# Kernel tuning notes

Hardware: AMD Instinct MI355X
Metric: run time of the kernel (lower is better)

## Reference

```python
import jax, jax.numpy as jnp
import numpy as np

N_NODES = 10000
N_EDGES = 160000
MUL = 128            # channel multiplicity
N_SPECIES = 4        # node_attrs scalars
N_RADIAL = 8         # edge_feats scalars
AVG_NEIGH = 16.0
SQRT3 = 1.7320508075688772


def setup_inputs() -> dict:
    key = jax.random.key(0)
    ks = jax.random.split(key, 16)
    inp = {}
    inp['node_attrs'] = jax.random.uniform(ks[0], (N_NODES, N_SPECIES), dtype=jnp.float32)
    inp['node_feats'] = jax.random.normal(ks[1], (N_NODES, MUL * 4), dtype=jnp.float32)  # 128x0e + 128x1o
    inp['edge_attrs'] = jax.random.normal(ks[2], (N_EDGES, 4), dtype=jnp.float32)        # 1x0e + 1x1o (SH lmax=1)
    inp['edge_feats'] = jax.random.normal(ks[3], (N_EDGES, N_RADIAL), dtype=jnp.float32)
    inp['edge_index'] = jax.random.randint(ks[4], (2, N_EDGES), 0, N_NODES, dtype=jnp.int32)
    # linear_up: per-l mixing (o3.Linear on 128x0e+128x1o)
    inp['W_up0'] = jax.random.normal(ks[5], (MUL, MUL), dtype=jnp.float32)
    inp['W_up1'] = jax.random.normal(ks[6], (MUL, MUL), dtype=jnp.float32)
    # radial MLP [8, 64, 64, 512] (conv_tp.weight_numel = 4 instructions * 128)
    inp['W_mlp1'] = jax.random.normal(ks[7], (N_RADIAL, 64), dtype=jnp.float32)
    inp['W_mlp2'] = jax.random.normal(ks[8], (64, 64), dtype=jnp.float32)
    inp['W_mlp3'] = jax.random.normal(ks[9], (64, 4 * MUL), dtype=jnp.float32)
    # linear: irreps_mid.simplify() = 256x0e + 256x1o -> 128x0e + 128x1o
    inp['W_lin0'] = jax.random.normal(ks[10], (2 * MUL, MUL), dtype=jnp.float32)
    inp['W_lin1'] = jax.random.normal(ks[11], (2 * MUL, MUL), dtype=jnp.float32)
    # skip_tp: FullyConnectedTensorProduct(target, 4x0e -> target), uvw weights per l
    inp['W_skip0'] = jax.random.normal(ks[12], (MUL, N_SPECIES, MUL), dtype=jnp.float32)
    inp['W_skip1'] = jax.random.normal(ks[13], (MUL, N_SPECIES, MUL), dtype=jnp.float32)
    inp['update_coeff_param'] = jnp.zeros((1,), dtype=jnp.float32)
    return inp


def reference(node_attrs, node_feats, edge_attrs, edge_feats, edge_index,
              W_up0, W_up1, W_mlp1, W_mlp2, W_mlp3, W_lin0, W_lin1,
              W_skip0, W_skip1, update_coeff_param):
    N = node_feats.shape[0]
    # split node feats into irrep blocks: scalars [N,128], vectors [N,128,3]
    s = node_feats[:, :MUL]
    v = node_feats[:, MUL:].reshape(N, MUL, 3)
    # linear_up (o3.Linear, fan-in normalized)
    inv_up = 1.0 / jnp.sqrt(jnp.float32(MUL))
    s = (s @ W_up0) * inv_up
    v = jnp.einsum('nui,uw->nwi', v, W_up1) * inv_up
    # radial MLP -> per-edge TP weights (e3nn FullyConnectedNet style, fan-in normalized, silu)
    h = jax.nn.silu((edge_feats @ W_mlp1) / jnp.sqrt(jnp.float32(N_RADIAL)))
    h = jax.nn.silu((h @ W_mlp2) / jnp.sqrt(jnp.float32(64)))
    tpw = (h @ W_mlp3) / jnp.sqrt(jnp.float32(64))  # [E, 512]
    # instruction order (sorted by output irrep): 0e*0e->0e, 1o*1o->0e, 0e*1o->1o, 1o*0e->1o
    w_a, w_b, w_c, w_d = tpw[:, :MUL], tpw[:, MUL:2*MUL], tpw[:, 2*MUL:3*MUL], tpw[:, 3*MUL:]
    sender, receiver = edge_index[0], edge_index[1]
    xs = s[sender]          # [E,128] gather
    xv = v[sender]          # [E,128,3]
    ea_s = edge_attrs[:, :1]    # [E,1]
    ea_v = edge_attrs[:, 1:4]   # [E,3]
    # CG tensor-product messages ('uvu', component norm)
    m0 = w_a * xs * ea_s                                        # 0e x 0e -> 0e
    m1 = w_b * (jnp.einsum('eui,ei->eu', xv, ea_v) / SQRT3)      # 1o x 1o -> 0e
    m2 = (w_c * xs)[:, :, None] * ea_v[:, None, :]               # 0e x 1o -> 1o
    m3 = w_d[:, :, None] * xv * ea_s[:, :, None]                 # 1o x 0e -> 1o
    ms = jnp.concatenate([m0, m1], axis=1)                       # [E,256]
    mv = jnp.concatenate([m2, m3], axis=1)                       # [E,256,3]
    # scatter-sum to receiver nodes
    Ms = jax.ops.segment_sum(ms, receiver, num_segments=N)       # [N,256]
    Mv = jax.ops.segment_sum(mv, receiver, num_segments=N)       # [N,256,3]
    # linear (256x0e+256x1o -> 128x0e+128x1o), divided by avg_num_neighbors
    inv_lin = 1.0 / (jnp.sqrt(jnp.float32(2 * MUL)) * AVG_NEIGH)
    S = (Ms @ W_lin0) * inv_lin                                  # [N,128]
    V = jnp.einsum('nui,uw->nwi', Mv, W_lin1) * inv_lin          # [N,128,3]
    # skip_tp: FullyConnectedTensorProduct(message, node_attrs) with uvw weights
    inv_sk = 1.0 / jnp.sqrt(jnp.float32(MUL * N_SPECIES))
    sc_s = jnp.einsum('nu,nv,uvw->nw', S, node_attrs, W_skip0) * inv_sk
    sc_v = jnp.einsum('nui,nv,uvw->nwi', V, node_attrs, W_skip1) * inv_sk
    # residual stream mixing (sc=False branch)
    c = jax.nn.sigmoid(update_coeff_param)                       # [1]
    c_old = jax.lax.rsqrt(c * c + 1.0)
    c_new = c * c_old
    S = c_old * S + c_new * sc_s
    V = c_old * V + c_new * sc_v
    # reshape_irreps: [N, mul, 1 + 3]
    out = jnp.concatenate([S[:, :, None], V], axis=-1)           # [N,128,4]
    return out
```

## Files before the change

### kernel.cpp

```cpp
#include <hip/hip_runtime.h>

#define MUL 128

typedef __attribute__((ext_vector_type(8))) short bf16x8;
typedef __attribute__((ext_vector_type(4))) short bf16x4;
typedef __attribute__((ext_vector_type(4))) float f32x4;

__device__ __constant__ float kINV_UP   = 0.08838834764831845f;
__device__ __constant__ float kINV_L1   = 0.35355339059327373f;
__device__ __constant__ float kINV_L2   = 0.125f;
__device__ __constant__ float kINV_L3   = 0.125f;
__device__ __constant__ float kINV_LIN  = 0.00390625f;
__device__ __constant__ float kINV_SK   = 0.044194173824159216f;
__device__ __constant__ float kINV_SQ3  = 0.5773502691896258f;

static __device__ __forceinline__ short f2bf(float f) {
  unsigned u = __float_as_uint(f);
  unsigned r = (u + 0x7FFFu + ((u >> 16) & 1u)) >> 16;
  return (short)r;
}

__global__ __launch_bounds__(256) void k_cvt(
    const float* __restrict__ W_up0, const float* __restrict__ W_up1,
    const float* __restrict__ W_lin0, const float* __restrict__ W_lin1,
    const float* __restrict__ W_sk0, const float* __restrict__ W_sk1,
    const float* __restrict__ W_mlp2, const float* __restrict__ W_mlp3,
    short* __restrict__ W0T, short* __restrict__ W1T,
    short* __restrict__ Wl0T, short* __restrict__ Wl1T,
    short* __restrict__ Wsk0T, short* __restrict__ Wsk1T,
    short* __restrict__ W2T, short* __restrict__ W3T) {
  int id = blockIdx.x * 256 + threadIdx.x;
  if (id < 16384) {
    int w = id >> 7, u = id & 127;
    W0T[id] = f2bf(W_up0[u * 128 + w]);
    return;
  }
  id -= 16384;
  if (id < 16384) {
    int w = id >> 7, u = id & 127;
    W1T[id] = f2bf(W_up1[u * 128 + w]);
    return;
  }
  id -= 16384;
  if (id < 32768) {
    int w = id >> 8, u = id & 255;
    Wl0T[id] = f2bf(W_lin0[u * 128 + w]);
    return;
  }
  id -= 32768;
  if (id < 32768) {
    int w = id >> 8, u = id & 255;
    Wl1T[id] = f2bf(W_lin1[u * 128 + w]);
    return;
  }
  id -= 32768;
  if (id < 65536) {
    int w = id >> 9, k = id & 511;
    int v = k >> 7, u = k & 127;
    Wsk0T[id] = f2bf(W_sk0[(u * 4 + v) * 128 + w]);
    return;
  }
  id -= 65536;
  if (id < 65536) {
    int w = id >> 9, k = id & 511;
    int v = k >> 7, u = k & 127;
    Wsk1T[id] = f2bf(W_sk1[(u * 4 + v) * 128 + w]);
    return;
  }
  id -= 65536;
  if (id < 4096) {
    int c = id >> 6, k = id & 63;
    W2T[id] = f2bf(W_mlp2[k * 64 + c]);
    return;
  }
  id -= 4096;
  if (id < 32768) {
    int c = id >> 6, k = id & 63;
    W3T[id] = f2bf(W_mlp3[k * 512 + c]);
  }
}

__global__ __launch_bounds__(256) void k_up_mfma(const float* __restrict__ nf,
                                                 const short* __restrict__ W0T,
                                                 const short* __restrict__ W1T,
                                                 float* __restrict__ s_up,
                                                 float* __restrict__ v_up,
                                                 int N) {
  __shared__ __align__(16) short lsA[4][16][136];
  const int nb = blockIdx.x * 16;
  const int t = threadIdx.x;

  for (int base = t * 8; base < 16 * 512; base += 256 * 8) {
    int n = base >> 9, j0 = base & 511;
    float vals[8];
    if (nb + n < N) {
      float4 q0 = *reinterpret_cast<const float4*>(nf + (size_t)(nb + n) * 512 + j0);
      float4 q1 = *reinterpret_cast<const float4*>(nf + (size_t)(nb + n) * 512 + j0 + 4);
      vals[0] = q0.x; vals[1] = q0.y; vals[2] = q0.z; vals[3] = q0.w;
      vals[4] = q1.x; vals[5] = q1.y; vals[6] = q1.z; vals[7] = q1.w;
    } else {
#pragma unroll
      for (int e = 0; e < 8; ++e) vals[e] = 0.f;
    }
#pragma unroll
    for (int e = 0; e < 8; ++e) {
      int idx = j0 + e;
      if (idx < 128) {
        lsA[0][n][idx] = f2bf(vals[e]);
      } else {
        unsigned q = idx - 128;
        unsigned u = q / 3u;
        unsigned i = q - u * 3u;
        lsA[1 + i][n][u] = f2bf(vals[e]);
      }
    }
  }
  __syncthreads();

  const int c = t >> 6;
  const int lane = t & 63;
  const int col = lane & 15;
  const int g = lane >> 4;

  const short* WT = c ? W1T : W0T;

  bf16x8 af[4];
#pragma unroll
  for (int kk = 0; kk < 4; ++kk)
    af[kk] = *reinterpret_cast<const bf16x8*>(&lsA[c][col][kk * 32 + g * 8]);

#pragma unroll
  for (int nt = 0; nt < 8; ++nt) {
    f32x4 acc = {0.f, 0.f, 0.f, 0.f};
#pragma unroll
    for (int kk = 0; kk < 4; ++kk) {
      bf16x8 bf = *reinterpret_cast<const bf16x8*>(&WT[(size_t)(nt * 16 + col) * 128 + kk * 32 + g * 8]);
      acc = __builtin_amdgcn_mfma_f32_16x16x32_bf16(af[kk], bf, acc, 0, 0, 0);
    }
#pragma unroll
    for (int r = 0; r < 4; ++r) {
      int nd = nb + g * 4 + r;
      if (nd < N) {
        float val = acc[r] * kINV_UP;
        if (c == 0) s_up[(size_t)nd * 128 + nt * 16 + col] = val;
        else        v_up[(size_t)nd * 384 + (c - 1) * 128 + nt * 16 + col] = val;
      }
    }
  }
}

__global__ void k_count(const int* __restrict__ eidx, int* __restrict__ cnt, int E) {
  int e = blockIdx.x * 256 + threadIdx.x;
  if (e < E) atomicAdd(&cnt[eidx[E + e]], 1);
}

__global__ __launch_bounds__(1024) void k_scan(const int* __restrict__ cnt,
                                               int* __restrict__ offs,
                                               int* __restrict__ cursor, int N) {
  __shared__ int part[1024];
  const int t = threadIdx.x;
  int CH = (N + 1023) >> 10;
  if (CH > 16) CH = 16;
  const int base = t * CH;
  int loc[16];
  int s = 0;
  for (int i = 0; i < CH; ++i) {
    int idx = base + i;
    loc[i] = (idx < N) ? cnt[idx] : 0;
    s += loc[i];
  }
  part[t] = s;
  __syncthreads();
  for (int off = 1; off < 1024; off <<= 1) {
    int v = part[t];
    int add = (t >= off) ? part[t - off] : 0;
    __syncthreads();
    part[t] = v + add;
    __syncthreads();
  }
  int excl = part[t] - s;
  for (int i = 0; i < CH; ++i) {
    int idx = base + i;
    if (idx < N) { offs[idx] = excl; cursor[idx] = excl; }
    excl += loc[i];
  }
  if (t == 1023) offs[N] = part[1023];
}

__global__ void k_scatter(const int* __restrict__ eidx, int* __restrict__ cursor,
                          int* __restrict__ sorted, int E) {
  int e = blockIdx.x * 256 + threadIdx.x;
  if (e < E) {
    int r = eidx[E + e];
    int p = atomicAdd(&cursor[r], 1);
    sorted[p] = e;
  }
}

__global__ __launch_bounds__(256) void k_mlp(
    const int* __restrict__ sorted, const float* __restrict__ ef,
    const float* __restrict__ W1, const short* __restrict__ W2T,
    const short* __restrict__ W3T, unsigned* __restrict__ tpw2, int E) {
  __shared__ float sef[64][12];
  __shared__ float sW1[8 * 64];
  __shared__ __align__(16) short sW2T[64][72];
  __shared__ __align__(16) short sh1[64][72];
  __shared__ __align__(16) short sh2[64][72];

  const int pb = blockIdx.x * 64;
  const int t = threadIdx.x;

  for (int i = t * 4; i < 512; i += 1024)
    *reinterpret_cast<float4*>(&sW1[i]) = *reinterpret_cast<const float4*>(W1 + i);
  for (int i = t * 8; i < 4096; i += 2048) {
    int r = i >> 6, c = i & 63;
    *reinterpret_cast<bf16x8*>(&sW2T[r][c]) = *reinterpret_cast<const bf16x8*>(&W2T[r * 64 + c]);
  }
  if (t < 128) {
    int le = t >> 1, half = t & 1;
    int p = pb + le;
    float4 q = {0.f, 0.f, 0.f, 0.f};
    if (p < E) {
      int eid = sorted[p];
      q = *reinterpret_cast<const float4*>(ef + (size_t)eid * 8 + half * 4);
    }
    *reinterpret_cast<float4*>(&sef[le][half * 4]) = q;
  }
  __syncthreads();

  {
    const int e = t & 63, cg = t >> 6;
    float acc[16] = {};
#pragma unroll
    for (int k = 0; k < 8; ++k) {
      float x = sef[e][k];
#pragma unroll
      for (int j = 0; j < 16; ++j) acc[j] += x * sW1[k * 64 + cg * 16 + j];
    }
#pragma unroll
    for (int j = 0; j < 16; ++j) {
      float a = acc[j] * kINV_L1;
      sh1[e][cg * 16 + j] = f2bf(a / (1.f + __expf(-a)));
    }
  }
  __syncthreads();

  const int lane = t & 63, w = t >> 6;
  const int li = lane & 15, g = lane >> 4;
  const int e = w * 16 + li;

  {
    bf16x8 b0 = *reinterpret_cast<const bf16x8*>(&sh1[e][g * 8]);
    bf16x8 b1 = *reinterpret_cast<const bf16x8*>(&sh1[e][32 + g * 8]);
#pragma unroll
    for (int ct = 0; ct < 4; ++ct) {
      bf16x8 a0 = *reinterpret_cast<const bf16x8*>(&sW2T[ct * 16 + li][g * 8]);
      bf16x8 a1 = *reinterpret_cast<const bf16x8*>(&sW2T[ct * 16 + li][32 + g * 8]);
      f32x4 acc = {0.f, 0.f, 0.f, 0.f};
      acc = __builtin_amdgcn_mfma_f32_16x16x32_bf16(a0, b0, acc, 0, 0, 0);
      acc = __builtin_amdgcn_mfma_f32_16x16x32_bf16(a1, b1, acc, 0, 0, 0);
      bf16x4 h;
#pragma unroll
      for (int r = 0; r < 4; ++r) {
        float a = acc[r] * kINV_L2;
        h[r] = f2bf(a / (1.f + __expf(-a)));
      }
      *reinterpret_cast<bf16x4*>(&sh2[e][ct * 16 + g * 4]) = h;
    }
  }
  __syncthreads();

  {
    const int p = pb + e;
    bf16x8 b0 = *reinterpret_cast<const bf16x8*>(&sh2[e][g * 8]);
    bf16x8 b1 = *reinterpret_cast<const bf16x8*>(&sh2[e][32 + g * 8]);
#pragma unroll 4
    for (int rt = 0; rt < 16; ++rt) {
      const int rowA = rt * 16 + li;
      bf16x8 a0 = *reinterpret_cast<const bf16x8*>(&W3T[(size_t)rowA * 64 + g * 8]);
      bf16x8 a1 = *reinterpret_cast<const bf16x8*>(&W3T[(size_t)rowA * 64 + 32 + g * 8]);
      bf16x8 a2 = *reinterpret_cast<const bf16x8*>(&W3T[(size_t)(rowA + 256) * 64 + g * 8]);
      bf16x8 a3 = *reinterpret_cast<const bf16x8*>(&W3T[(size_t)(rowA + 256) * 64 + 32 + g * 8]);
      f32x4 accA = {0.f, 0.f, 0.f, 0.f};
      f32x4 accB = {0.f, 0.f, 0.f, 0.f};
      accA = __builtin_amdgcn_mfma_f32_16x16x32_bf16(a0, b0, accA, 0, 0, 0);
      accA = __builtin_amdgcn_mfma_f32_16x16x32_bf16(a1, b1, accA, 0, 0, 0);
      accB = __builtin_amdgcn_mfma_f32_16x16x32_bf16(a2, b0, accB, 0, 0, 0);
      accB = __builtin_amdgcn_mfma_f32_16x16x32_bf16(a3, b1, accB, 0, 0, 0);
      if (p < E) {
        uint4 d;
        unsigned* dp = &d.x;
#pragma unroll
        for (int r = 0; r < 4; ++r) {
          unsigned lo = (unsigned)(unsigned short)f2bf(accA[r] * kINV_L3);
          unsigned hi = (unsigned)(unsigned short)f2bf(accB[r] * kINV_L3);
          dp[r] = lo | (hi << 16);
        }
        *reinterpret_cast<uint4*>(&tpw2[(size_t)p * 256 + rt * 16 + g * 4]) = d;
      }
    }
  }
}

__global__ __launch_bounds__(256) void k_gather(
    const int* __restrict__ sorted, const int* __restrict__ offs,
    const unsigned* __restrict__ tpw2, const float* __restrict__ eattr,
    const int* __restrict__ eidx,
    const float* __restrict__ s_up, const float* __restrict__ v_up,
    float* __restrict__ Ms, float* __restrict__ Mv, int N, int SB) {
  const int t = threadIdx.x;
  const int vside = blockIdx.x >= SB;
  const int nb = (vside ? blockIdx.x - SB : blockIdx.x) * 4;
  const int n = nb + (t >> 6);
  if (n >= N) return;
  const int l = t & 63;
  const int u0 = l * 2;

  float aMs0 = 0.f, aMs1 = 0.f;
  float aV[3][2] = {};

  const int e0 = offs[n], e1 = offs[n + 1];

  if (!vside) {
    for (int p = e0; p < e1; ++p) {
      int eid = sorted[p];
      int snd = eidx[eid];
      float4 ea = *reinterpret_cast<const float4*>(eattr + (size_t)eid * 4);
      uint2 q = *reinterpret_cast<const uint2*>(tpw2 + (size_t)p * 256 + u0);
      float2 xs = *reinterpret_cast<const float2*>(s_up + (size_t)snd * 128 + u0);
      float tA0 = __uint_as_float(q.x << 16);
      float tB0 = __uint_as_float(q.x & 0xFFFF0000u);
      float tA1 = __uint_as_float(q.y << 16);
      float tB1 = __uint_as_float(q.y & 0xFFFF0000u);
      float xe0 = xs.x * ea.x, xe1 = xs.y * ea.x;
      aMs0 += tA0 * xe0;
      aMs1 += tA1 * xe1;
      float wc0 = tB0 * xs.x, wc1 = tB1 * xs.y;
      aV[0][0] += wc0 * ea.y; aV[0][1] += wc1 * ea.y;
      aV[1][0] += wc0 * ea.z; aV[1][1] += wc1 * ea.z;
      aV[2][0] += wc0 * ea.w; aV[2][1] += wc1 * ea.w;
    }
    *reinterpret_cast<float2*>(Ms + (size_t)n * 256 + u0) = make_float2(aMs0, aMs1);
#pragma unroll
    for (int i = 0; i < 3; ++i)
      *reinterpret_cast<float2*>(Mv + (size_t)n * 768 + i * 256 + u0) =
          make_float2(aV[i][0], aV[i][1]);
  } else {
    for (int p = e0; p < e1; ++p) {
      int eid = sorted[p];
      int snd = eidx[eid];
      float4 ea = *reinterpret_cast<const float4*>(eattr + (size_t)eid * 4);
      uint2 q = *reinterpret_cast<const uint2*>(tpw2 + (size_t)p * 256 + 128 + u0);
      const float* xv = v_up + (size_t)snd * 384 + u0;
      float2 x0 = *reinterpret_cast<const float2*>(xv);
      float2 x1 = *reinterpret_cast<const float2*>(xv + 128);
      float2 x2 = *reinterpret_cast<const float2*>(xv + 256);
      float tA0 = __uint_as_float(q.x << 16);
      float tB0 = __uint_as_float(q.x & 0xFFFF0000u);
      float tA1 = __uint_as_float(q.y << 16);
      float tB1 = __uint_as_float(q.y & 0xFFFF0000u);
      float dot0 = x0.x * ea.y + x1.x * ea.z + x2.x * ea.w;
      float dot1 = x0.y * ea.y + x1.y * ea.z + x2.y * ea.w;
      aMs0 += tA0 * dot0 * kINV_SQ3;
      aMs1 += tA1 * dot1 * kINV_SQ3;
      float wd0 = tB0 * ea.x, wd1 = tB1 * ea.x;
      aV[0][0] += wd0 * x0.x; aV[0][1] += wd1 * x0.y;
      aV[1][0] += wd0 * x1.x; aV[1][1] += wd1 * x1.y;
      aV[2][0] += wd0 * x2.x; aV[2][1] += wd1 * x2.y;
    }
    *reinterpret_cast<float2*>(Ms + (size_t)n * 256 + 128 + u0) = make_float2(aMs0, aMs1);
#pragma unroll
    for (int i = 0; i < 3; ++i)
      *reinterpret_cast<float2*>(Mv + (size_t)n * 768 + i * 256 + 128 + u0) =
          make_float2(aV[i][0], aV[i][1]);
  }
}

__global__ __launch_bounds__(256) void k_linskip(
    const float* __restrict__ Ms, const float* __restrict__ Mv,
    const short* __restrict__ Wl0T, const short* __restrict__ Wl1T,
    const short* __restrict__ Wsk0T, const short* __restrict__ Wsk1T,
    const float* __restrict__ attrs, const float* __restrict__ upd,
    float* __restrict__ out, int N) {
  __shared__ __align__(16) short lsA[4][16][264];
  __shared__ __align__(16) short lsS[4][16][136];
  __shared__ float sat[16][4];
  const int nb = blockIdx.x * 16;
  const int t = threadIdx.x;

  for (int base = t * 4; base < 16 * 1024; base += 1024) {
    int n = base >> 10, j = base & 1023;
    int comp = j >> 8, u = j & 255;
    float4 q = {0.f, 0.f, 0.f, 0.f};
    if (nb + n < N) {
      const float* src = (comp == 0) ? (Ms + (size_t)(nb + n) * 256 + u)
                                     : (Mv + (size_t)(nb + n) * 768 + (size_t)(comp - 1) * 256 + u);
      q = *reinterpret_cast<const float4*>(src);
    }
    lsA[comp][n][u + 0] = f2bf(q.x);
    lsA[comp][n][u + 1] = f2bf(q.y);
    lsA[comp][n][u + 2] = f2bf(q.z);
    lsA[comp][n][u + 3] = f2bf(q.w);
  }
  if (t < 64) {
    int n = t >> 2, v = t & 3;
    sat[n][v] = (nb + n < N) ? attrs[(size_t)(nb + n) * 4 + v] : 0.f;
  }
  __syncthreads();

  const int c = t >> 6;
  const int lane = t & 63;
  const int col = lane & 15;
  const int g = lane >> 4;

  const short* WLT = c ? Wl1T : Wl0T;
  const short* WST = c ? Wsk1T : Wsk0T;

  bf16x8 af1[8];
#pragma unroll
  for (int kk = 0; kk < 8; ++kk)
    af1[kk] = *reinterpret_cast<const bf16x8*>(&lsA[c][col][kk * 32 + g * 8]);

  f32x4 Sreg[8];
#pragma unroll
  for (int nt = 0; nt < 8; ++nt) {
    f32x4 acc = {0.f, 0.f, 0.f, 0.f};
#pragma unroll
    for (int kk = 0; kk < 8; ++kk) {
      bf16x8 bf = *reinterpret_cast<const bf16x8*>(&WLT[(size_t)(nt * 16 + col) * 256 + kk * 32 + g * 8]);
      acc = __builtin_amdgcn_mfma_f32_16x16x32_bf16(af1[kk], bf, acc, 0, 0, 0);
    }
#pragma unroll
    for (int r = 0; r < 4; ++r) acc[r] *= kINV_LIN;
    Sreg[nt] = acc;
#pragma unroll
    for (int r = 0; r < 4; ++r)
      lsS[c][g * 4 + r][nt * 16 + col] = f2bf(acc[r]);
  }

  float satr[4][4];
#pragma unroll
  for (int r = 0; r < 4; ++r)
#pragma unroll
    for (int v = 0; v < 4; ++v) satr[r][v] = sat[g * 4 + r][v];

  __syncthreads();

  bf16x8 af2[4];
#pragma unroll
  for (int kk = 0; kk < 4; ++kk)
    af2[kk] = *reinterpret_cast<const bf16x8*>(&lsS[c][col][kk * 32 + g * 8]);

  const float p = upd[0];
  const float cc = 1.f / (1.f + __expf(-p));
  const float c_old = rsqrtf(cc * cc + 1.f);
  const float c_new = cc * c_old;

#pragma unroll
  for (int nt = 0; nt < 8; ++nt) {
    float fin[4] = {0.f, 0.f, 0.f, 0.f};
#pragma unroll
    for (int v = 0; v < 4; ++v) {
      f32x4 tmp = {0.f, 0.f, 0.f, 0.f};
#pragma unroll
      for (int kk = 0; kk < 4; ++kk) {
        bf16x8 bf = *reinterpret_cast<const bf16x8*>(&WST[(size_t)(nt * 16 + col) * 512 + v * 128 + kk * 32 + g * 8]);
        tmp = __builtin_amdgcn_mfma_f32_16x16x32_bf16(af2[kk], bf, tmp, 0, 0, 0);
      }
#pragma unroll
      for (int r = 0; r < 4; ++r) fin[r] += satr[r][v] * tmp[r];
    }
#pragma unroll
    for (int r = 0; r < 4; ++r) {
      int nd = nb + g * 4 + r;
      if (nd < N) {
        float val = c_old * Sreg[nt][r] + c_new * fin[r] * kINV_SK;
        out[((size_t)nd * 128 + nt * 16 + col) * 4 + c] = val;
      }
    }
  }
}

extern "C" void kernel_launch(void* const* d_in, const int* in_sizes, int n_in,
                              void* d_out, int out_size, void* d_ws, size_t ws_size,
                              hipStream_t stream) {
  const float* node_attrs = (const float*)d_in[0];
  const float* node_feats = (const float*)d_in[1];
  const float* edge_attrs = (const float*)d_in[2];
  const float* edge_feats = (const float*)d_in[3];
  const int*   edge_index = (const int*)d_in[4];
  const float* W_up0  = (const float*)d_in[5];
  const float* W_up1  = (const float*)d_in[6];
  const float* W_mlp1 = (const float*)d_in[7];
  const float* W_mlp2 = (const float*)d_in[8];
  const float* W_mlp3 = (const float*)d_in[9];
  const float* W_lin0 = (const float*)d_in[10];
  const float* W_lin1 = (const float*)d_in[11];
  const float* W_skip0 = (const float*)d_in[12];
  const float* W_skip1 = (const float*)d_in[13];
  const float* upd = (const float*)d_in[14];
  float* out = (float*)d_out;

  const int N = in_sizes[0] / 4;
  const int E = in_sizes[4] / 2;

  float* ws = (float*)d_ws;
  float* s_up = ws;
  float* v_up = s_up + (size_t)N * 128;
  float* Ms   = v_up + (size_t)N * 384;
  float* Mv   = Ms + (size_t)N * 256;
  int* cnt    = (int*)(Mv + (size_t)N * 768);
  int* offs   = cnt + N;
  int* cursor = offs + N + 1;
  int* sorted = cursor + N;

  short* wbase = (short*)((((uintptr_t)(sorted + E)) + 15) & ~(uintptr_t)15);
  short* W0T   = wbase;
  short* W1T   = W0T + 16384;
  short* Wl0T  = W1T + 16384;
  short* Wl1T  = Wl0T + 32768;
  short* Wsk0T = Wl1T + 32768;
  short* Wsk1T = Wsk0T + 65536;
  short* W2T   = Wsk1T + 65536;
  short* W3T   = W2T + 4096;
  unsigned* tpw2 = (unsigned*)(W3T + 32768);

  hipMemsetAsync(cnt, 0, (size_t)N * sizeof(int), stream);

  k_cvt<<<(266240 + 255) / 256, 256, 0, stream>>>(W_up0, W_up1, W_lin0, W_lin1,
                                                  W_skip0, W_skip1, W_mlp2, W_mlp3,
                                                  W0T, W1T, Wl0T, Wl1T, Wsk0T, Wsk1T,
                                                  W2T, W3T);
  k_up_mfma<<<(N + 15) / 16, 256, 0, stream>>>(node_feats, W0T, W1T, s_up, v_up, N);
  k_count<<<(E + 255) / 256, 256, 0, stream>>>(edge_index, cnt, E);
  k_scan<<<1, 1024, 0, stream>>>(cnt, offs, cursor, N);
  k_scatter<<<(E + 255) / 256, 256, 0, stream>>>(edge_index, cursor, sorted, E);
  k_mlp<<<(E + 63) / 64, 256, 0, stream>>>(sorted, edge_feats, W_mlp1, W2T, W3T, tpw2, E);
  const int SB = (N + 3) / 4;
  k_gather<<<2 * SB, 256, 0, stream>>>(sorted, offs, tpw2, edge_attrs, edge_index,
                                       s_up, v_up, Ms, Mv, N, SB);
  k_linskip<<<(N + 15) / 16, 256, 0, stream>>>(Ms, Mv, Wl0T, Wl1T, Wsk0T, Wsk1T,
                                               node_attrs, upd, out, N);
}
```

Measured before the change: 327.2 us.

## Merge independent launches into horizontally fused kernels and index MLP output by edge

Merges weight conversion with edge counting into one launch, and merges the radial MLP, the up-projection and the CSR scatter into a single kernel whose blocks branch on their block index. The MLP now reads edge features and writes tpw2 in original edge order instead of sorted order, so it no longer depends on the sort. The gather then reads tpw2 by edge id, which makes those reads scattered rather than contiguous. Within-wave LDS waits replace block-wide barriers in the MLP, cutting launch count and serial dependencies between stages.

```diff
diff --git a/kernel.cpp b/kernel.cpp
--- a/kernel.cpp
+++ b/kernel.cpp
@@ -14,13 +14,15 @@
 __device__ __constant__ float kINV_SK   = 0.044194173824159216f;
 __device__ __constant__ float kINV_SQ3  = 0.5773502691896258f;
 
+#define WAVE_LDS_SYNC() asm volatile("s_waitcnt lgkmcnt(0)" ::: "memory")
+
 static __device__ __forceinline__ short f2bf(float f) {
   unsigned u = __float_as_uint(f);
   unsigned r = (u + 0x7FFFu + ((u >> 16) & 1u)) >> 16;
   return (short)r;
 }
 
-__global__ __launch_bounds__(256) void k_cvt(
+__global__ __launch_bounds__(256) void k_cvtcnt(
     const float* __restrict__ W_up0, const float* __restrict__ W_up1,
     const float* __restrict__ W_lin0, const float* __restrict__ W_lin1,
     const float* __restrict__ W_sk0, const float* __restrict__ W_sk1,
@@ -28,8 +30,15 @@
     short* __restrict__ W0T, short* __restrict__ W1T,
     short* __restrict__ Wl0T, short* __restrict__ Wl1T,
     short* __restrict__ Wsk0T, short* __restrict__ Wsk1T,
-    short* __restrict__ W2T, short* __restrict__ W3T) {
-  int id = blockIdx.x * 256 + threadIdx.x;
+    short* __restrict__ W2T, short* __restrict__ W3T,
+    const int* __restrict__ eidx, int* __restrict__ cnt, int E, int CVT_B) {
+  int blk = blockIdx.x;
+  if (blk >= CVT_B) {
+    int e = (blk - CVT_B) * 256 + threadIdx.x;
+    if (e < E) atomicAdd(&cnt[eidx[E + e]], 1);
+    return;
+  }
+  int id = blk * 256 + threadIdx.x;
   if (id < 16384) {
     int w = id >> 7, u = id & 127;
     W0T[id] = f2bf(W_up0[u * 128 + w]);
@@ -78,80 +87,6 @@
     int c = id >> 6, k = id & 63;
     W3T[id] = f2bf(W_mlp3[k * 512 + c]);
   }
-}
-
-__global__ __launch_bounds__(256) void k_up_mfma(const float* __restrict__ nf,
-                                                 const short* __restrict__ W0T,
-                                                 const short* __restrict__ W1T,
-                                                 float* __restrict__ s_up,
-                                                 float* __restrict__ v_up,
-                                                 int N) {
-  __shared__ __align__(16) short lsA[4][16][136];
-  const int nb = blockIdx.x * 16;
-  const int t = threadIdx.x;
-
-  for (int base = t * 8; base < 16 * 512; base += 256 * 8) {
-    int n = base >> 9, j0 = base & 511;
-    float vals[8];
-    if (nb + n < N) {
-      float4 q0 = *reinterpret_cast<const float4*>(nf + (size_t)(nb + n) * 512 + j0);
-      float4 q1 = *reinterpret_cast<const float4*>(nf + (size_t)(nb + n) * 512 + j0 + 4);
-      vals[0] = q0.x; vals[1] = q0.y; vals[2] = q0.z; vals[3] = q0.w;
-      vals[4] = q1.x; vals[5] = q1.y; vals[6] = q1.z; vals[7] = q1.w;
-    } else {
-#pragma unroll
-      for (int e = 0; e < 8; ++e) vals[e] = 0.f;
-    }
-#pragma unroll
-    for (int e = 0; e < 8; ++e) {
-      int idx = j0 + e;
-      if (idx < 128) {
-        lsA[0][n][idx] = f2bf(vals[e]);
-      } else {
-        unsigned q = idx - 128;
-        unsigned u = q / 3u;
-        unsigned i = q - u * 3u;
-        lsA[1 + i][n][u] = f2bf(vals[e]);
-      }
-    }
-  }
-  __syncthreads();
-
-  const int c = t >> 6;
-  const int lane = t & 63;
-  const int col = lane & 15;
-  const int g = lane >> 4;
-
-  const short* WT = c ? W1T : W0T;
-
-  bf16x8 af[4];
-#pragma unroll
-  for (int kk = 0; kk < 4; ++kk)
-    af[kk] = *reinterpret_cast<const bf16x8*>(&lsA[c][col][kk * 32 + g * 8]);
-
-#pragma unroll
-  for (int nt = 0; nt < 8; ++nt) {
-    f32x4 acc = {0.f, 0.f, 0.f, 0.f};
-#pragma unroll
-    for (int kk = 0; kk < 4; ++kk) {
-      bf16x8 bf = *reinterpret_cast<const bf16x8*>(&WT[(size_t)(nt * 16 + col) * 128 + kk * 32 + g * 8]);
-      acc = __builtin_amdgcn_mfma_f32_16x16x32_bf16(af[kk], bf, acc, 0, 0, 0);
-    }
-#pragma unroll
-    for (int r = 0; r < 4; ++r) {
-      int nd = nb + g * 4 + r;
-      if (nd < N) {
-        float val = acc[r] * kINV_UP;
-        if (c == 0) s_up[(size_t)nd * 128 + nt * 16 + col] = val;
-        else        v_up[(size_t)nd * 384 + (c - 1) * 128 + nt * 16 + col] = val;
-      }
-    }
-  }
-}
-
-__global__ void k_count(const int* __restrict__ eidx, int* __restrict__ cnt, int E) {
-  int e = blockIdx.x * 256 + threadIdx.x;
-  if (e < E) atomicAdd(&cnt[eidx[E + e]], 1);
 }
 
 __global__ __launch_bounds__(1024) void k_scan(const int* __restrict__ cnt,
@@ -187,118 +122,185 @@
   if (t == 1023) offs[N] = part[1023];
 }
 
-__global__ void k_scatter(const int* __restrict__ eidx, int* __restrict__ cursor,
-                          int* __restrict__ sorted, int E) {
-  int e = blockIdx.x * 256 + threadIdx.x;
+__global__ __launch_bounds__(256) void k_fused3(
+    const int* __restrict__ eidx, int* __restrict__ cursor, int* __restrict__ sorted,
+    const float* __restrict__ nf, const short* __restrict__ W0T,
+    const short* __restrict__ W1T, float* __restrict__ s_up, float* __restrict__ v_up,
+    const float* __restrict__ ef, const float* __restrict__ W1f,
+    const short* __restrict__ W2T, const short* __restrict__ W3T,
+    unsigned* __restrict__ tpw2, int N, int E, int MLP_B, int UP_B) {
+  __shared__ __align__(16) char smem[29696];
+  const int t = threadIdx.x;
+  int blk = blockIdx.x;
+
+  if (blk < MLP_B) {
+    float* sW1  = (float*)smem;
+    short* sW2T = (short*)(smem + 2048);
+    short* sh1  = (short*)(smem + 11264);
+    short* sh2  = (short*)(smem + 20480);
+
+    for (int i = t * 4; i < 512; i += 1024)
+      *reinterpret_cast<float4*>(&sW1[i]) = *reinterpret_cast<const float4*>(W1f + i);
+    for (int i = t * 8; i < 4096; i += 2048) {
+      int r = i >> 6, c = i & 63;
+      *reinterpret_cast<bf16x8*>(&sW2T[r * 72 + c]) =
+          *reinterpret_cast<const bf16x8*>(&W2T[r * 64 + c]);
+    }
+    __syncthreads();
+
+    const int w = t >> 6, l = t & 63, li = l & 15, g = l >> 4;
+    const int e = blk * 64 + w * 16 + li;
+    short* h1row = sh1 + (w * 16 + li) * 72;
+    short* h2row = sh2 + (w * 16 + li) * 72;
+
+    float4 qa = {0.f, 0.f, 0.f, 0.f}, qb = {0.f, 0.f, 0.f, 0.f};
+    if (e < E) {
+      qa = *reinterpret_cast<const float4*>(ef + (size_t)e * 8);
+      qb = *reinterpret_cast<const float4*>(ef + (size_t)e * 8 + 4);
+    }
+    const float x[8] = {qa.x, qa.y, qa.z, qa.w, qb.x, qb.y, qb.z, qb.w};
+    {
+      bf16x8 p0, p1;
+#pragma unroll
+      for (int j = 0; j < 16; ++j) {
+        int col = g * 16 + j;
+        float a = 0.f;
+#pragma unroll
+        for (int k = 0; k < 8; ++k) a += x[k] * sW1[k * 64 + col];
+        a *= kINV_L1;
+        short hv = f2bf(a / (1.f + __expf(-a)));
+        if (j < 8) p0[j] = hv; else p1[j - 8] = hv;
+      }
+      *reinterpret_cast<bf16x8*>(&h1row[g * 16])     = p0;
+      *reinterpret_cast<bf16x8*>(&h1row[g * 16 + 8]) = p1;
+    }
+    WAVE_LDS_SYNC();
+
+    {
+      bf16x8 b0 = *reinterpret_cast<const bf16x8*>(&h1row[g * 8]);
+      bf16x8 b1 = *reinterpret_cast<const bf16x8*>(&h1row[32 + g * 8]);
+#pragma unroll
+      for (int ct = 0; ct < 4; ++ct) {
+        const short* wrow = &sW2T[(ct * 16 + li) * 72];
+        bf16x8 a0 = *reinterpret_cast<const bf16x8*>(&wrow[g * 8]);
+        bf16x8 a1 = *reinterpret_cast<const bf16x8*>(&wrow[32 + g * 8]);
+        f32x4 acc = {0.f, 0.f, 0.f, 0.f};
+        acc = __builtin_amdgcn_mfma_f32_16x16x32_bf16(a0, b0, acc, 0, 0, 0);
+        acc = __builtin_amdgcn_mfma_f32_16x16x32_bf16(a1, b1, acc, 0, 0, 0);
+        bf16x4 hq;
+#pragma unroll
+        for (int r = 0; r < 4; ++r) {
+          float a = acc[r] * kINV_L2;
+          hq[r] = f2bf(a / (1.f + __expf(-a)));
+        }
+        *reinterpret_cast<bf16x4*>(&h2row[ct * 16 + g * 4]) = hq;
+      }
+    }
+    WAVE_LDS_SYNC();
+
+    {
+      bf16x8 b0 = *reinterpret_cast<const bf16x8*>(&h2row[g * 8]);
+      bf16x8 b1 = *reinterpret_cast<const bf16x8*>(&h2row[32 + g * 8]);
+#pragma unroll 4
+      for (int rt = 0; rt < 16; ++rt) {
+        const int rowA = rt * 16 + li;
+        bf16x8 a0 = *reinterpret_cast<const bf16x8*>(&W3T[(size_t)rowA * 64 + g * 8]);
+        bf16x8 a1 = *reinterpret_cast<const bf16x8*>(&W3T[(size_t)rowA * 64 + 32 + g * 8]);
+        bf16x8 a2 = *reinterpret_cast<const bf16x8*>(&W3T[(size_t)(rowA + 256) * 64 + g * 8]);
+        bf16x8 a3 = *reinterpret_cast<const bf16x8*>(&W3T[(size_t)(rowA + 256) * 64 + 32 + g * 8]);
+        f32x4 accA = {0.f, 0.f, 0.f, 0.f};
+        f32x4 accB = {0.f, 0.f, 0.f, 0.f};
+        accA = __builtin_amdgcn_mfma_f32_16x16x32_bf16(a0, b0, accA, 0, 0, 0);
+        accA = __builtin_amdgcn_mfma_f32_16x16x32_bf16(a1, b1, accA, 0, 0, 0);
+        accB = __builtin_amdgcn_mfma_f32_16x16x32_bf16(a2, b0, accB, 0, 0, 0);
+        accB = __builtin_amdgcn_mfma_f32_16x16x32_bf16(a3, b1, accB, 0, 0, 0);
+        if (e < E) {
+          uint4 d;
+          unsigned* dp = &d.x;
+#pragma unroll
+          for (int r = 0; r < 4; ++r) {
+            unsigned lo = (unsigned)(unsigned short)f2bf(accA[r] * kINV_L3);
+            unsigned hi = (unsigned)(unsigned short)f2bf(accB[r] * kINV_L3);
+            dp[r] = lo | (hi << 16);
+          }
+          *reinterpret_cast<uint4*>(&tpw2[(size_t)e * 256 + rt * 16 + g * 4]) = d;
+        }
+      }
+    }
+    return;
+  }
+  blk -= MLP_B;
+
+  if (blk < UP_B) {
+    short* lsA = (short*)smem;
+    const int nb = blk * 16;
+
+    for (int base = t * 8; base < 16 * 512; base += 256 * 8) {
+      int n = base >> 9, j0 = base & 511;
+      float vals[8];
+      if (nb + n < N) {
+        float4 q0 = *reinterpret_cast<const float4*>(nf + (size_t)(nb + n) * 512 + j0);
+        float4 q1 = *reinterpret_cast<const float4*>(nf + (size_t)(nb + n) * 512 + j0 + 4);
+        vals[0] = q0.x; vals[1] = q0.y; vals[2] = q0.z; vals[3] = q0.w;
+        vals[4] = q1.x; vals[5] = q1.y; vals[6] = q1.z; vals[7] = q1.w;
+      } else {
+#pragma unroll
+        for (int e = 0; e < 8; ++e) vals[e] = 0.f;
+      }
+#pragma unroll
+      for (int e = 0; e < 8; ++e) {
+        int idx = j0 + e;
+        if (idx < 128) {
+          lsA[(0 * 16 + n) * 136 + idx] = f2bf(vals[e]);
+        } else {
+          unsigned q = idx - 128;
+          unsigned u = q / 3u;
+          unsigned i = q - u * 3u;
+          lsA[((1 + i) * 16 + n) * 136 + u] = f2bf(vals[e]);
+        }
+      }
+    }
+    __syncthreads();
+
+    const int c = t >> 6;
+    const int lane = t & 63;
+    const int col = lane & 15;
+    const int g = lane >> 4;
+
+    const short* WT = c ? W1T : W0T;
+
+    bf16x8 af[4];
+#pragma unroll
+    for (int kk = 0; kk < 4; ++kk)
+      af[kk] = *reinterpret_cast<const bf16x8*>(&lsA[(c * 16 + col) * 136 + kk * 32 + g * 8]);
+
+#pragma unroll
+    for (int nt = 0; nt < 8; ++nt) {
+      f32x4 acc = {0.f, 0.f, 0.f, 0.f};
+#pragma unroll
+      for (int kk = 0; kk < 4; ++kk) {
+        bf16x8 bf = *reinterpret_cast<const bf16x8*>(&WT[(size_t)(nt * 16 + col) * 128 + kk * 32 + g * 8]);
+        acc = __builtin_amdgcn_mfma_f32_16x16x32_bf16(af[kk], bf, acc, 0, 0, 0);
+      }
+#pragma unroll
+      for (int r = 0; r < 4; ++r) {
+        int nd = nb + g * 4 + r;
+        if (nd < N) {
+          float val = acc[r] * kINV_UP;
+          if (c == 0) s_up[(size_t)nd * 128 + nt * 16 + col] = val;
+          else        v_up[(size_t)nd * 384 + (c - 1) * 128 + nt * 16 + col] = val;
+        }
+      }
+    }
+    return;
+  }
+  blk -= UP_B;
+
+  int e = blk * 256 + t;
   if (e < E) {
     int r = eidx[E + e];
     int p = atomicAdd(&cursor[r], 1);
     sorted[p] = e;
-  }
-}
-
-__global__ __launch_bounds__(256) void k_mlp(
-    const int* __restrict__ sorted, const float* __restrict__ ef,
-    const float* __restrict__ W1, const short* __restrict__ W2T,
-    const short* __restrict__ W3T, unsigned* __restrict__ tpw2, int E) {
-  __shared__ float sef[64][12];
-  __shared__ float sW1[8 * 64];
-  __shared__ __align__(16) short sW2T[64][72];
-  __shared__ __align__(16) short sh1[64][72];
-  __shared__ __align__(16) short sh2[64][72];
-
-  const int pb = blockIdx.x * 64;
-  const int t = threadIdx.x;
-
-  for (int i = t * 4; i < 512; i += 1024)
-    *reinterpret_cast<float4*>(&sW1[i]) = *reinterpret_cast<const float4*>(W1 + i);
-  for (int i = t * 8; i < 4096; i += 2048) {
-    int r = i >> 6, c = i & 63;
-    *reinterpret_cast<bf16x8*>(&sW2T[r][c]) = *reinterpret_cast<const bf16x8*>(&W2T[r * 64 + c]);
-  }
-  if (t < 128) {
-    int le = t >> 1, half = t & 1;
-    int p = pb + le;
-    float4 q = {0.f, 0.f, 0.f, 0.f};
-    if (p < E) {
-      int eid = sorted[p];
-      q = *reinterpret_cast<const float4*>(ef + (size_t)eid * 8 + half * 4);
-    }
-    *reinterpret_cast<float4*>(&sef[le][half * 4]) = q;
-  }
-  __syncthreads();
-
-  {
-    const int e = t & 63, cg = t >> 6;
-    float acc[16] = {};
-#pragma unroll
-    for (int k = 0; k < 8; ++k) {
-      float x = sef[e][k];
-#pragma unroll
-      for (int j = 0; j < 16; ++j) acc[j] += x * sW1[k * 64 + cg * 16 + j];
-    }
-#pragma unroll
-    for (int j = 0; j < 16; ++j) {
-      float a = acc[j] * kINV_L1;
-      sh1[e][cg * 16 + j] = f2bf(a / (1.f + __expf(-a)));
-    }
-  }
-  __syncthreads();
-
-  const int lane = t & 63, w = t >> 6;
-  const int li = lane & 15, g = lane >> 4;
-  const int e = w * 16 + li;
-
-  {
-    bf16x8 b0 = *reinterpret_cast<const bf16x8*>(&sh1[e][g * 8]);
-    bf16x8 b1 = *reinterpret_cast<const bf16x8*>(&sh1[e][32 + g * 8]);
-#pragma unroll
-    for (int ct = 0; ct < 4; ++ct) {
-      bf16x8 a0 = *reinterpret_cast<const bf16x8*>(&sW2T[ct * 16 + li][g * 8]);
-      bf16x8 a1 = *reinterpret_cast<const bf16x8*>(&sW2T[ct * 16 + li][32 + g * 8]);
-      f32x4 acc = {0.f, 0.f, 0.f, 0.f};
-      acc = __builtin_amdgcn_mfma_f32_16x16x32_bf16(a0, b0, acc, 0, 0, 0);
-      acc = __builtin_amdgcn_mfma_f32_16x16x32_bf16(a1, b1, acc, 0, 0, 0);
-      bf16x4 h;
-#pragma unroll
-      for (int r = 0; r < 4; ++r) {
-        float a = acc[r] * kINV_L2;
-        h[r] = f2bf(a / (1.f + __expf(-a)));
-      }
-      *reinterpret_cast<bf16x4*>(&sh2[e][ct * 16 + g * 4]) = h;
-    }
-  }
-  __syncthreads();
-
-  {
-    const int p = pb + e;
-    bf16x8 b0 = *reinterpret_cast<const bf16x8*>(&sh2[e][g * 8]);
-    bf16x8 b1 = *reinterpret_cast<const bf16x8*>(&sh2[e][32 + g * 8]);
-#pragma unroll 4
-    for (int rt = 0; rt < 16; ++rt) {
-      const int rowA = rt * 16 + li;
-      bf16x8 a0 = *reinterpret_cast<const bf16x8*>(&W3T[(size_t)rowA * 64 + g * 8]);
-      bf16x8 a1 = *reinterpret_cast<const bf16x8*>(&W3T[(size_t)rowA * 64 + 32 + g * 8]);
-      bf16x8 a2 = *reinterpret_cast<const bf16x8*>(&W3T[(size_t)(rowA + 256) * 64 + g * 8]);
-      bf16x8 a3 = *reinterpret_cast<const bf16x8*>(&W3T[(size_t)(rowA + 256) * 64 + 32 + g * 8]);
-      f32x4 accA = {0.f, 0.f, 0.f, 0.f};
-      f32x4 accB = {0.f, 0.f, 0.f, 0.f};
-      accA = __builtin_amdgcn_mfma_f32_16x16x32_bf16(a0, b0, accA, 0, 0, 0);
-      accA = __builtin_amdgcn_mfma_f32_16x16x32_bf16(a1, b1, accA, 0, 0, 0);
-      accB = __builtin_amdgcn_mfma_f32_16x16x32_bf16(a2, b0, accB, 0, 0, 0);
-      accB = __builtin_amdgcn_mfma_f32_16x16x32_bf16(a3, b1, accB, 0, 0, 0);
-      if (p < E) {
-        uint4 d;
-        unsigned* dp = &d.x;
-#pragma unroll
-        for (int r = 0; r < 4; ++r) {
-          unsigned lo = (unsigned)(unsigned short)f2bf(accA[r] * kINV_L3);
-          unsigned hi = (unsigned)(unsigned short)f2bf(accB[r] * kINV_L3);
-          dp[r] = lo | (hi << 16);
-        }
-        *reinterpret_cast<uint4*>(&tpw2[(size_t)p * 256 + rt * 16 + g * 4]) = d;
-      }
-    }
   }
 }
 
@@ -326,7 +328,7 @@
       int eid = sorted[p];
       int snd = eidx[eid];
       float4 ea = *reinterpret_cast<const float4*>(eattr + (size_t)eid * 4);
-      uint2 q = *reinterpret_cast<const uint2*>(tpw2 + (size_t)p * 256 + u0);
+      uint2 q = *reinterpret_cast<const uint2*>(tpw2 + (size_t)eid * 256 + u0);
       float2 xs = *reinterpret_cast<const float2*>(s_up + (size_t)snd * 128 + u0);
       float tA0 = __uint_as_float(q.x << 16);
       float tB0 = __uint_as_float(q.x & 0xFFFF0000u);
@@ -350,7 +352,7 @@
       int eid = sorted[p];
       int snd = eidx[eid];
       float4 ea = *reinterpret_cast<const float4*>(eattr + (size_t)eid * 4);
-      uint2 q = *reinterpret_cast<const uint2*>(tpw2 + (size_t)p * 256 + 128 + u0);
+      uint2 q = *reinterpret_cast<const uint2*>(tpw2 + (size_t)eid * 256 + 128 + u0);
       const float* xv = v_up + (size_t)snd * 384 + u0;
       float2 x0 = *reinterpret_cast<const float2*>(xv);
       float2 x1 = *reinterpret_cast<const float2*>(xv + 128);
@@ -525,18 +527,24 @@
   short* W3T   = W2T + 4096;
   unsigned* tpw2 = (unsigned*)(W3T + 32768);
 
+  const int CVT_B = (266240 + 255) / 256;
+  const int CNT_B = (E + 255) / 256;
+  const int MLP_B = (E + 63) / 64;
+  const int UP_B  = (N + 15) / 16;
+  const int SC_B  = (E + 255) / 256;
+  const int SB    = (N + 3) / 4;
+
   hipMemsetAsync(cnt, 0, (size_t)N * sizeof(int), stream);
 
-  k_cvt<<<(266240 + 255) / 256, 256, 0, stream>>>(W_up0, W_up1, W_lin0, W_lin1,
-                                                  W_skip0, W_skip1, W_mlp2, W_mlp3,
-                                                  W0T, W1T, Wl0T, Wl1T, Wsk0T, Wsk1T,
-                                                  W2T, W3T);
-  k_up_mfma<<<(N + 15) / 16, 256, 0, stream>>>(node_feats, W0T, W1T, s_up, v_up, N);
-  k_count<<<(E + 255) / 256, 256, 0, stream>>>(edge_index, cnt, E);
+  k_cvtcnt<<<CVT_B + CNT_B, 256, 0, stream>>>(
+      W_up0, W_up1, W_lin0, W_lin1, W_skip0, W_skip1, W_mlp2, W_mlp3,
+      W0T, W1T, Wl0T, Wl1T, Wsk0T, Wsk1T, W2T, W3T,
+      edge_index, cnt, E, CVT_B);
   k_scan<<<1, 1024, 0, stream>>>(cnt, offs, cursor, N);
-  k_scatter<<<(E + 255) / 256, 256, 0, stream>>>(edge_index, cursor, sorted, E);
-  k_mlp<<<(E + 63) / 64, 256, 0, stream>>>(sorted, edge_feats, W_mlp1, W2T, W3T, tpw2, E);
-  const int SB = (N + 3) / 4;
+  k_fused3<<<MLP_B + UP_B + SC_B, 256, 0, stream>>>(
+      edge_index, cursor, sorted,
+      node_feats, W0T, W1T, s_up, v_up,
+      edge_feats, W_mlp1, W2T, W3T, tpw2, N, E, MLP_B, UP_B);
   k_gather<<<2 * SB, 256, 0, stream>>>(sorted, offs, tpw2, edge_attrs, edge_index,
                                        s_up, v_up, Ms, Mv, N, SB);
   k_linskip<<<(N + 15) / 16, 256, 0, stream>>>(Ms, Mv, Wl0T, Wl1T, Wsk0T, Wsk1T,
```

Result: faster. 316.8 us (-3.2%).
